# Kernel optimization log

Hardware: AMD Instinct MI355X
Metric: run time of the kernel (lower is better)

Reference implementation:

```python
import jax, jax.numpy as jnp
import numpy as np


def setup_inputs() -> dict:
    key = jax.random.key(0)
    ks = jax.random.split(key, 4)
    B, C, H, W, L = 2, 32, 128, 128, 7
    return {
        "x": jax.random.normal(ks[0], (B, C, H, W), jnp.float32),
        # conv3d3x3: Conv3d(C, 32, (1,3,3)) -> 2D conv weight [32, C, 3, 3]
        "w1": jax.random.normal(ks[1], (32, C, 3, 3), jnp.float32) * 0.05,
        "b1": jnp.zeros((32,), jnp.float32),
        # conv3d1x1: Conv3d(32, 1, 1) -> pointwise weight [1, 32]
        "w2": jax.random.normal(ks[2], (1, 32), jnp.float32) * 0.05,
        "b2": jnp.zeros((1,), jnp.float32),
        # conv3d9x9x1: Conv3d(C, C, (1,L,L)) -> weight [C, C, L, L]
        "w3": jax.random.normal(ks[3], (C, C, L, L), jnp.float32) * 0.02,
        "b3": jnp.zeros((C,), jnp.float32),
        "local_scale": 7,
    }


def reference(x, w1, b1, w2, b2, w3, b3, local_scale):
    # sliding_window branch of Local_attention.forward
    L = int(local_scale)
    pad = L // 2
    B, C, H, W = x.shape
    P = H * W
    # F.unfold with kernel (H, W) and padding=pad over padded input gives the
    # L*L shifted copies of the full feature map. Equivalent gather:
    # local_x[b,c,ki*W+kj,wi,wj] = x_pad[b,c, ki+wi, kj+wj]
    xp = jnp.pad(x, ((0, 0), (0, 0), (pad, pad), (pad, pad)))
    local = jnp.stack(
        [xp[:, :, wi:wi + H, wj:wj + W] for wi in range(L) for wj in range(L)],
        axis=-1,
    )  # [B, C, H, W, L*L]
    local = local.reshape(B, C, P, L, L)
    # Conv3d kernels with depth-size 1 act independently per depth slice ->
    # fold the depth (pixel) dim into the batch and run 2D convs.
    lx = local.transpose(0, 2, 1, 3, 4).reshape(B * P, C, L, L)
    k = jax.lax.conv_general_dilated(
        lx, w1, window_strides=(1, 1), padding=((1, 1), (1, 1)),
        dimension_numbers=("NCHW", "OIHW", "NCHW"),
    ) + b1[None, :, None, None]                      # [B*P, 32, L, L]
    att = jax.nn.sigmoid(
        jnp.einsum("nchw,oc->nohw", k, w2) + b2[None, :, None, None]
    )                                                # [B*P, 1, L, L]
    att_x = lx * att + lx                            # gated residual
    # Conv3d(C, C, (1,L,L)) valid -> full contraction over (C_in, L, L)
    out = jnp.einsum("nchw,ochw->no", att_x, w3) + b3  # [B*P, C]
    output = out.reshape(B, P, C).transpose(0, 2, 1).reshape(B, C, H, W)
    att_mp = att.reshape(B, P, 1, L, L).transpose(0, 2, 1, 3, 4)  # [B,1,P,L,L]
    return output, att_mp
```

## Files before the change

### kernel.cpp

```cpp
#include <hip/hip_runtime.h>
#include <math.h>

typedef __attribute__((ext_vector_type(8))) short bf16x8;
typedef __attribute__((ext_vector_type(4))) float f32x4;
typedef __attribute__((ext_vector_type(4))) unsigned int u32x4;
typedef __attribute__((ext_vector_type(2))) unsigned int u32x2;

namespace {
constexpr int OUT0 = 2 * 32 * 16384;
}

__device__ __forceinline__ unsigned int bf16_rne(float f) {
  unsigned int u = __builtin_bit_cast(unsigned int, f);
  return u + 0x7fffu + ((u >> 16) & 1u);
}
__device__ __forceinline__ unsigned int bf16_rhu(float f) {
  return __builtin_bit_cast(unsigned int, f) + 0x8000u;
}
__device__ __forceinline__ unsigned int pack_rne(float lo, float hi) {
  return __builtin_amdgcn_perm(bf16_rne(hi), bf16_rne(lo), 0x07060302u);
}
__device__ __forceinline__ unsigned int pack_rhu(float lo, float hi) {
  return __builtin_amdgcn_perm(bf16_rhu(hi), bf16_rhu(lo), 0x07060302u);
}
__device__ __forceinline__ float bf16_to_f32(unsigned int u16v) {
  return __builtin_bit_cast(float, u16v << 16);
}

__global__ __launch_bounds__(256) void prep_kernel(
    const float* __restrict__ w1, const float* __restrict__ b1,
    const float* __restrict__ w2, const float* __restrict__ b2,
    const float* __restrict__ w3,
    float* __restrict__ wk, unsigned int* __restrict__ w3f) {
  int t = threadIdx.x, blk = blockIdx.x;
  if (blk < 98) {
    int f = blk * 256 + t;
    int d = f & 3;
    int lane = (f >> 2) & 63;
    int nt = (f >> 8) & 1;
    int ij = f >> 9;
    int o = nt * 16 + (lane & 15);
    int k0 = ((lane >> 4) << 3) + 2 * d;
    float f0 = w3[o * 1568 + k0 * 49 + ij];
    float f1 = w3[o * 1568 + (k0 + 1) * 49 + ij];
    w3f[f] = pack_rne(f0, f1);
  } else {
    int k = (blk - 98) * 256 + t;
    if (k < 288) {
      int c = k / 9, r = k - c * 9;
      float s = 0.f;
#pragma unroll
      for (int o = 0; o < 32; ++o) s += w2[o] * w1[o * 288 + c * 9 + r];
      wk[k] = s;
    } else if (k == 288) {
      float s = b2[0];
#pragma unroll
      for (int o = 0; o < 32; ++o) s += w2[o] * b1[o];
      wk[288] = s;
    }
  }
}

__global__ __launch_bounds__(512, 4) void fused_kernel(
    const float* __restrict__ x, const float* __restrict__ wk,
    const unsigned int* __restrict__ w3f, const float* __restrict__ b3,
    float* __restrict__ out, float* __restrict__ att_out) {
  __shared__ __align__(16) char regA[16384];
  unsigned short* xs16 = (unsigned short*)regA;
  float* as_ = (float*)regA;
  __shared__ __align__(16) unsigned short xh[224 * 40];
  __shared__ unsigned short ysb[9 * 224];
  __shared__ float wks[289];

  int t = threadIdx.x;
  int bi = blockIdx.x;
  int b = bi >> 8;
  int tile = bi & 255;
  int y0 = (tile >> 4) << 3, x0 = (tile & 15) << 3;
  const float* xb = x + ((long)b << 19);

  for (int k = t; k < 289; k += 512) wks[k] = wk[k];

#pragma unroll
  for (int it = 0; it < 4; ++it) {
    int idx = it * 512 + t;
    int c = idx >> 6;
    int r64 = idx & 63;
    int row = r64 >> 2, seg = r64 & 3;
    int gy = y0 + row - 4;
    int gxs = x0 + (seg << 2) - 4;
    f32x4 v = {0.f, 0.f, 0.f, 0.f};
    if ((unsigned)gy < 128u && (unsigned)gxs < 128u)
      v = *reinterpret_cast<const f32x4*>(xb + (c << 14) + (gy << 7) + gxs);
    u32x2 p;
    p[0] = pack_rhu(v[0], v[1]);
    p[1] = pack_rhu(v[2], v[3]);
    *reinterpret_cast<u32x2*>(reinterpret_cast<unsigned int*>(xs16) +
                              (c << 7) + (r64 << 1)) = p;
  }
  __syncthreads();

  if (t < 256) {
    int r = t >> 4;
    bool inner = (unsigned)(r - 1) < 14u;
    int n = t - 16;
    unsigned int u[32];
#pragma unroll
    for (int c = 0; c < 32; ++c) u[c] = xs16[(c << 8) + t];
    float s[9];
#pragma unroll
    for (int dd = 0; dd < 9; ++dd) s[dd] = 0.f;
#pragma unroll
    for (int c = 0; c < 32; ++c) {
      float xf = bf16_to_f32(u[c]);
#pragma unroll
      for (int dd = 0; dd < 9; ++dd) s[dd] += xf * wks[c * 9 + dd];
    }
    if (inner) {
#pragma unroll
      for (int dd = 0; dd < 9; ++dd)
        ysb[dd * 224 + n] = (unsigned short)(bf16_rhu(s[dd]) >> 16);
      unsigned int* xhd = reinterpret_cast<unsigned int*>(xh) + n * 20;
#pragma unroll
      for (int g4 = 0; g4 < 4; ++g4) {
        u32x4 d;
#pragma unroll
        for (int e = 0; e < 4; ++e) {
          int k2 = g4 * 4 + e;
          d[e] = __builtin_amdgcn_perm(u[2 * k2 + 1], u[2 * k2], 0x05040100u);
        }
        *reinterpret_cast<u32x4*>(xhd + g4 * 4) = d;
      }
    }
  }
  __syncthreads();

#pragma unroll 1
  for (int it = 0; it < 7; ++it) {
    int f = it * 512 + t;
    if (f < 3136) {
      int pos = f >> 6;
      int px = f & 63;
      int py = px >> 3, pxl = px & 7;
      int i = pos / 7, j = pos - i * 7;
      float s = wks[288];
#pragma unroll
      for (int di = 0; di < 3; ++di) {
        int ii = i + di - 1;
        if ((unsigned)ii >= 7u) continue;
#pragma unroll
        for (int dj = 0; dj < 3; ++dj) {
          int jj = j + dj - 1;
          if ((unsigned)jj >= 7u) continue;
          s += bf16_to_f32(
              (unsigned int)ysb[(di * 3 + dj) * 224 + (py + ii) * 16 + pxl + jj + 1]);
        }
      }
      as_[pos * 68 + px] = 1.f + 1.f / (1.f + expf(-s));
    }
  }
  __syncthreads();

#pragma unroll 1
  for (int it = 0; it < 7; ++it) {
    int f = it * 512 + t;
    if (f < 3136) {
      int row = f / 392;
      int rem = f - row * 392;
      int pxl = rem / 49;
      int pos = rem - pxl * 49;
      long base = ((long)(b << 14) + ((y0 + row) << 7) + x0) * 49;
      att_out[base + rem] = as_[pos * 68 + (row << 3) + pxl] - 1.f;
    }
  }

  int wv = t >> 6, lane = t & 63;
  int mt = wv >> 1, oh = wv & 1;
  int ml = lane & 15, q = lane >> 4;
  int px = mt * 16 + ml;
  int py = px >> 3, pxl = px & 7;
  f32x4 acc = {0.f, 0.f, 0.f, 0.f};
  const u32x4* bp = reinterpret_cast<const u32x4*>(w3f) + lane + oh * 64;
#pragma unroll 1
  for (int i = 0; i < 7; ++i) {
    int nb = (py + i) * 16 + pxl + 1;
#pragma unroll
    for (int j = 0; j < 7; ++j) {
      int ij = i * 7 + j;
      u32x4 bw = bp[ij * 128];
      bf16x8 af = *reinterpret_cast<const bf16x8*>(&xh[(nb + j) * 40 + (q << 3)]);
      f32x4 gv = *reinterpret_cast<const f32x4*>(&as_[ij * 68 + mt * 16 + (q << 2)]);
      f32x4 z = {0.f, 0.f, 0.f, 0.f};
      f32x4 P = __builtin_amdgcn_mfma_f32_16x16x32_bf16(
          af, __builtin_bit_cast(bf16x8, bw), z, 0, 0, 0);
#pragma unroll
      for (int r = 0; r < 4; ++r) acc[r] += gv[r] * P[r];
    }
  }
  __syncthreads();

  {
    int o = oh * 16 + ml;
    float bv = b3[o];
#pragma unroll
    for (int r = 0; r < 4; ++r)
      as_[o * 68 + mt * 16 + (q << 2) + r] = acc[r] + bv;
  }
  __syncthreads();
#pragma unroll
  for (int rep = 0; rep < 4; ++rep) {
    int idx = rep * 512 + t;
    int o = idx >> 6, pxs = idx & 63;
    out[((long)b << 19) + (o << 14) + ((y0 + (pxs >> 3)) << 7) + x0 + (pxs & 7)]
        = as_[o * 68 + pxs];
  }
}

extern "C" void kernel_launch(void* const* d_in, const int* in_sizes, int n_in,
                              void* d_out, int out_size, void* d_ws, size_t ws_size,
                              hipStream_t stream) {
  const float* x  = (const float*)d_in[0];
  const float* w1 = (const float*)d_in[1];
  const float* b1 = (const float*)d_in[2];
  const float* w2 = (const float*)d_in[3];
  const float* b2 = (const float*)d_in[4];
  const float* w3 = (const float*)d_in[5];
  const float* b3 = (const float*)d_in[6];

  float* out = (float*)d_out;
  float* att_out = out + OUT0;
  float* wk = (float*)d_ws;
  unsigned int* w3f = (unsigned int*)((char*)d_ws + 4096);

  prep_kernel<<<100, 256, 0, stream>>>(w1, b1, w2, b2, w3, wk, w3f);
  fused_kernel<<<512, 512, 0, stream>>>(x, wk, w3f, b3, out, att_out);
}
```

Before: 89.07 us.

## Fold weight prep into fused kernel with flag-based cross-block sync

Removes the separate prep kernel launch. The first 49 blocks repack w3 into the MFMA layout and publish per-block magic flags, and every block spins on those flags before its MFMA phase. Each block also computes the collapsed w1·w2 weights itself in shared memory. The MFMA work is re-split so each wave computes both output halves over alternating taps, with a two-phase reduction through LDS. The sigmoid now uses fast exp and rcp intrinsics. The spin-wait assumes the producer blocks are co-resident, and magic flag values left in the workspace from earlier runs could be accepted as stale.

```diff
diff --git a/kernel.cpp b/kernel.cpp
--- a/kernel.cpp
+++ b/kernel.cpp
@@ -1,5 +1,4 @@
 #include <hip/hip_runtime.h>
-#include <math.h>
 
 typedef __attribute__((ext_vector_type(8))) short bf16x8;
 typedef __attribute__((ext_vector_type(4))) float f32x4;
@@ -27,44 +26,17 @@
   return __builtin_bit_cast(float, u16v << 16);
 }
 
-__global__ __launch_bounds__(256) void prep_kernel(
-    const float* __restrict__ w1, const float* __restrict__ b1,
-    const float* __restrict__ w2, const float* __restrict__ b2,
-    const float* __restrict__ w3,
-    float* __restrict__ wk, unsigned int* __restrict__ w3f) {
-  int t = threadIdx.x, blk = blockIdx.x;
-  if (blk < 98) {
-    int f = blk * 256 + t;
-    int d = f & 3;
-    int lane = (f >> 2) & 63;
-    int nt = (f >> 8) & 1;
-    int ij = f >> 9;
-    int o = nt * 16 + (lane & 15);
-    int k0 = ((lane >> 4) << 3) + 2 * d;
-    float f0 = w3[o * 1568 + k0 * 49 + ij];
-    float f1 = w3[o * 1568 + (k0 + 1) * 49 + ij];
-    w3f[f] = pack_rne(f0, f1);
-  } else {
-    int k = (blk - 98) * 256 + t;
-    if (k < 288) {
-      int c = k / 9, r = k - c * 9;
-      float s = 0.f;
-#pragma unroll
-      for (int o = 0; o < 32; ++o) s += w2[o] * w1[o * 288 + c * 9 + r];
-      wk[k] = s;
-    } else if (k == 288) {
-      float s = b2[0];
-#pragma unroll
-      for (int o = 0; o < 32; ++o) s += w2[o] * b1[o];
-      wk[288] = s;
-    }
-  }
+__device__ __forceinline__ unsigned int flag_magic(int i) {
+  return 0x5F3C9A71u + (unsigned int)i * 0x9E3779B9u;
 }
 
 __global__ __launch_bounds__(512, 4) void fused_kernel(
-    const float* __restrict__ x, const float* __restrict__ wk,
-    const unsigned int* __restrict__ w3f, const float* __restrict__ b3,
-    float* __restrict__ out, float* __restrict__ att_out) {
+    const float* __restrict__ x, const float* __restrict__ w1,
+    const float* __restrict__ b1, const float* __restrict__ w2,
+    const float* __restrict__ b2, const float* __restrict__ w3,
+    const float* __restrict__ b3, unsigned int* __restrict__ w3f,
+    unsigned int* __restrict__ flags, float* __restrict__ out,
+    float* __restrict__ att_out) {
   __shared__ __align__(16) char regA[16384];
   unsigned short* xs16 = (unsigned short*)regA;
   float* as_ = (float*)regA;
@@ -79,7 +51,39 @@
   int y0 = (tile >> 4) << 3, x0 = (tile & 15) << 3;
   const float* xb = x + ((long)b << 19);
 
-  for (int k = t; k < 289; k += 512) wks[k] = wk[k];
+  {
+    int f = bi * 512 + t;
+    if (f < 25088) {
+      int d = f & 3;
+      int lane = (f >> 2) & 63;
+      int nt = (f >> 8) & 1;
+      int ij = f >> 9;
+      int o = nt * 16 + (lane & 15);
+      int k0 = ((lane >> 4) << 3) + 2 * d;
+      float f0 = w3[o * 1568 + k0 * 49 + ij];
+      float f1 = w3[o * 1568 + (k0 + 1) * 49 + ij];
+      w3f[f] = pack_rne(f0, f1);
+    }
+  }
+
+  if (t < 288) {
+    float s = 0.f;
+#pragma unroll
+    for (int o = 0; o < 32; ++o) s += w2[o] * w1[o * 288 + t];
+    wks[t] = s;
+  } else if (t == 288) {
+    float s = b2[0];
+#pragma unroll
+    for (int o = 0; o < 32; ++o) s += w2[o] * b1[o];
+    wks[288] = s;
+  }
+  __syncthreads();
+
+  if (bi < 49 && t == 0) {
+    __threadfence();
+    __hip_atomic_store(&flags[bi], flag_magic(bi), __ATOMIC_RELEASE,
+                       __HIP_MEMORY_SCOPE_AGENT);
+  }
 
 #pragma unroll
   for (int it = 0; it < 4; ++it) {
@@ -156,7 +160,8 @@
               (unsigned int)ysb[(di * 3 + dj) * 224 + (py + ii) * 16 + pxl + jj + 1]);
         }
       }
-      as_[pos * 68 + px] = 1.f + 1.f / (1.f + expf(-s));
+      float e = __expf(-s);
+      as_[pos * 68 + px] = 1.f + __builtin_amdgcn_rcpf(1.f + e);
     }
   }
   __syncthreads();
@@ -174,37 +179,69 @@
     }
   }
 
+  if (t < 49) {
+    unsigned int want = flag_magic(t);
+    while (__hip_atomic_load(&flags[t], __ATOMIC_ACQUIRE,
+                             __HIP_MEMORY_SCOPE_AGENT) != want) {}
+  }
+  __threadfence();
+  __syncthreads();
+
   int wv = t >> 6, lane = t & 63;
-  int mt = wv >> 1, oh = wv & 1;
+  int mt = wv >> 1, th = wv & 1;
   int ml = lane & 15, q = lane >> 4;
   int px = mt * 16 + ml;
   int py = px >> 3, pxl = px & 7;
-  f32x4 acc = {0.f, 0.f, 0.f, 0.f};
-  const u32x4* bp = reinterpret_cast<const u32x4*>(w3f) + lane + oh * 64;
-#pragma unroll 1
-  for (int i = 0; i < 7; ++i) {
-    int nb = (py + i) * 16 + pxl + 1;
-#pragma unroll
-    for (int j = 0; j < 7; ++j) {
-      int ij = i * 7 + j;
-      u32x4 bw = bp[ij * 128];
-      bf16x8 af = *reinterpret_cast<const bf16x8*>(&xh[(nb + j) * 40 + (q << 3)]);
-      f32x4 gv = *reinterpret_cast<const f32x4*>(&as_[ij * 68 + mt * 16 + (q << 2)]);
-      f32x4 z = {0.f, 0.f, 0.f, 0.f};
-      f32x4 P = __builtin_amdgcn_mfma_f32_16x16x32_bf16(
-          af, __builtin_bit_cast(bf16x8, bw), z, 0, 0, 0);
-#pragma unroll
-      for (int r = 0; r < 4; ++r) acc[r] += gv[r] * P[r];
-    }
+  f32x4 acc0 = {0.f, 0.f, 0.f, 0.f};
+  f32x4 acc1 = {0.f, 0.f, 0.f, 0.f};
+  const u32x4* bp = reinterpret_cast<const u32x4*>(w3f) + lane;
+  auto tap = [&](int ij) {
+    int i = (ij * 37) >> 8;
+    int j = ij - i * 7;
+    int nb = (py + i) * 16 + pxl + 1 + j;
+    u32x4 bw0 = bp[ij * 128];
+    u32x4 bw1 = bp[ij * 128 + 64];
+    bf16x8 af = *reinterpret_cast<const bf16x8*>(&xh[nb * 40 + (q << 3)]);
+    f32x4 gv = *reinterpret_cast<const f32x4*>(&as_[ij * 68 + mt * 16 + (q << 2)]);
+    f32x4 z = {0.f, 0.f, 0.f, 0.f};
+    f32x4 P0 = __builtin_amdgcn_mfma_f32_16x16x32_bf16(
+        af, __builtin_bit_cast(bf16x8, bw0), z, 0, 0, 0);
+    f32x4 P1 = __builtin_amdgcn_mfma_f32_16x16x32_bf16(
+        af, __builtin_bit_cast(bf16x8, bw1), z, 0, 0, 0);
+#pragma unroll
+    for (int r = 0; r < 4; ++r) {
+      acc0[r] += gv[r] * P0[r];
+      acc1[r] += gv[r] * P1[r];
+    }
+  };
+  if (th == 0) {
+#pragma unroll 3
+    for (int k = 0; k < 25; ++k) tap(2 * k);
+  } else {
+#pragma unroll 3
+    for (int k = 0; k < 24; ++k) tap(2 * k + 1);
   }
   __syncthreads();
 
   {
-    int o = oh * 16 + ml;
-    float bv = b3[o];
-#pragma unroll
-    for (int r = 0; r < 4; ++r)
-      as_[o * 68 + mt * 16 + (q << 2) + r] = acc[r] + bv;
+    int o0 = ml, o1 = 16 + ml;
+    int base = mt * 16 + (q << 2);
+    if (th == 0) {
+      float bv0 = b3[o0], bv1 = b3[o1];
+#pragma unroll
+      for (int r = 0; r < 4; ++r) {
+        as_[o0 * 68 + base + r] = acc0[r] + bv0;
+        as_[o1 * 68 + base + r] = acc1[r] + bv1;
+      }
+    }
+    __syncthreads();
+    if (th == 1) {
+#pragma unroll
+      for (int r = 0; r < 4; ++r) {
+        as_[o0 * 68 + base + r] += acc0[r];
+        as_[o1 * 68 + base + r] += acc1[r];
+      }
+    }
   }
   __syncthreads();
 #pragma unroll
@@ -229,9 +266,9 @@
 
   float* out = (float*)d_out;
   float* att_out = out + OUT0;
-  float* wk = (float*)d_ws;
+  unsigned int* flags = (unsigned int*)d_ws;
   unsigned int* w3f = (unsigned int*)((char*)d_ws + 4096);
 
-  prep_kernel<<<100, 256, 0, stream>>>(w1, b1, w2, b2, w3, wk, w3f);
-  fused_kernel<<<512, 512, 0, stream>>>(x, wk, w3f, b3, out, att_out);
-}
+  fused_kernel<<<512, 512, 0, stream>>>(x, w1, b1, w2, b2, w3, b3, w3f, flags,
+                                        out, att_out);
+}
```

Measured after the change: 179.3 us. 2.01x slower.
